# Kernel tuning notes

Hardware: AMD Instinct MI355X
Metric: run time of the kernel (lower is better)

## Reference

```python
import jax, jax.numpy as jnp
import numpy as np

U = 8192        # unique source nodes this hop
E = 200000      # candidate paths (edges)
D = 768         # node feature dim (== hidden, GIN residual requires it)
DE = 50         # edge one-hot dim
O = 768         # output dim
BN_EPS = 1e-5


def setup_inputs() -> dict:
    key = jax.random.key(0)
    ks = jax.random.split(key, 10)
    inp = {
        "x_src_unique": jax.random.normal(ks[0], (U, D), dtype=jnp.float32),
        "unique_src_to_process_indices": jnp.arange(U, dtype=jnp.int64),
        "path_source_indices_global": jax.random.randint(ks[1], (E,), 0, U).astype(jnp.int64),
        "path_target_node_features": jax.random.normal(ks[2], (E, D), dtype=jnp.float32),
        "path_edge_features": jax.random.normal(ks[3], (E, DE), dtype=jnp.float32),
        # edge_transform_linear: Linear(D+DE, H) with bias
        "W_edge": jax.random.normal(ks[4], (D, D + DE), dtype=jnp.float32) * (1.0 / np.sqrt(D + DE)),
        "b_edge": jnp.zeros((D,), dtype=jnp.float32),
        # MLP: two bias-free linears with BatchNorm1d between
        "W1": jax.random.normal(ks[5], (D, D), dtype=jnp.float32) * (1.0 / np.sqrt(D)),
        "W2": jax.random.normal(ks[6], (O, D), dtype=jnp.float32) * (1.0 / np.sqrt(D)),
        "bn_gamma": jnp.ones((D,), dtype=jnp.float32),
        "bn_beta": jnp.zeros((D,), dtype=jnp.float32),
        "eps_param": jnp.zeros((1,), dtype=jnp.float32),  # GIN eps (init_eps=0)
    }
    return inp


def reference(x_src_unique, unique_src_to_process_indices, path_source_indices_global,
              path_target_node_features, path_edge_features,
              W_edge, b_edge, W1, W2, bn_gamma, bn_beta, eps_param):
    # map global source ids -> local rows of x_src_unique (unique ids are sorted)
    local_idx = jnp.searchsorted(unique_src_to_process_indices, path_source_indices_global)

    # per-path message: relu(Linear([h_tgt ; e_onehot]))  -> [E, H]
    msg_in = jnp.concatenate([path_target_node_features, path_edge_features], axis=-1)
    msgs = jax.nn.relu(msg_in @ W_edge.T + b_edge)

    # scatter-sum messages to their source node  -> [U, H]
    agg = jax.ops.segment_sum(msgs, local_idx, num_segments=x_src_unique.shape[0])

    # GIN combine + MLP (BatchNorm1d in training mode, batch > 1)
    h = (1.0 + eps_param[0]) * x_src_unique + agg
    h1 = h @ W1.T                               # [U, H]
    mean = jnp.mean(h1, axis=0)
    var = jnp.var(h1, axis=0)                   # biased, matches torch BN normalization
    h1 = (h1 - mean) * jax.lax.rsqrt(var + BN_EPS) * bn_gamma + bn_beta
    h1 = jax.nn.relu(h1)
    return h1 @ W2.T                            # [U, O]
```

## Files before the change

kernel.cpp:

```cpp
#include <hip/hip_runtime.h>
#include <stdint.h>
#include <math.h>

typedef unsigned short u16;
typedef __attribute__((ext_vector_type(4))) float f32x4;
typedef __attribute__((ext_vector_type(8))) short s16x8;
typedef __attribute__((ext_vector_type(4))) int i32x4;

#define U_N 8192
#define E_N 200000
#define M_PAD 200192
#define D_N 768
#define DE_N 50
#define KP_E 832
#define NTI 13
#define BN_EPS 1e-5f

__device__ __forceinline__ u16 f2bf(float f) {
  union { float f; unsigned u; } v; v.f = f;
  return (u16)((v.u + 0x7fffu + ((v.u >> 16) & 1u)) >> 16);
}
__device__ __forceinline__ float bf2f(u16 v) {
  union { unsigned u; float f; } x; x.u = ((unsigned)v) << 16; return x.f;
}
__device__ __forceinline__ void gload16(const void* g, void* l) {
  __builtin_amdgcn_global_load_lds((const __attribute__((address_space(1))) void*)g,
                                   (__attribute__((address_space(3))) void*)l, 16, 0, 0);
}

__global__ void k_localidx(const int* __restrict__ uniq, const int* __restrict__ src,
                           int* __restrict__ lidx) {
  int e = blockIdx.x * 256 + threadIdx.x;
  if (e >= E_N) return;
  int v = src[e];
  int lo = 0, hi = U_N;
  while (lo < hi) { int mid = (lo + hi) >> 1; if (uniq[mid] < v) lo = mid + 1; else hi = mid; }
  lidx[e] = lo;
}

__global__ void k_hist(const int* __restrict__ lidx, int* __restrict__ counts) {
  int e = blockIdx.x * 256 + threadIdx.x;
  if (e < E_N) atomicAdd(&counts[lidx[e]], 1);
}

__global__ void k_scan(const int* __restrict__ counts, int* __restrict__ starts) {
  __shared__ int part[1024];
  const int t = threadIdx.x;
  const int base = t * 8;
  int loc[8]; int s = 0;
#pragma unroll
  for (int i = 0; i < 8; i++) { loc[i] = s; s += counts[base + i]; }
  part[t] = s; __syncthreads();
  for (int off = 1; off < 1024; off <<= 1) {
    int v = (t >= off) ? part[t - off] : 0;
    __syncthreads();
    part[t] += v;
    __syncthreads();
  }
  const int pre = (t == 0) ? 0 : part[t - 1];
#pragma unroll
  for (int i = 0; i < 8; i++) starts[base + i] = pre + loc[i];
  if (t == 1023) starts[8192] = pre + s;
}

__global__ void k_scatter(const int* __restrict__ lidx, const int* __restrict__ starts,
                          int* __restrict__ cursor, int* __restrict__ eord,
                          int* __restrict__ nsort) {
  int e = blockIdx.x * 256 + threadIdx.x;
  if (e >= E_N) return;
  int u = lidx[e];
  int pos = atomicAdd(&cursor[u], 1);
  eord[starts[u] + pos] = e;
  nsort[starts[u] + pos] = u;
}

__global__ __launch_bounds__(256)
void k_pack_q8(const float* __restrict__ tgt, const float* __restrict__ edg,
               const int* __restrict__ eord, char* __restrict__ Aq,
               float* __restrict__ sA) {
  const int row = blockIdx.x * 4 + (threadIdx.x >> 6);
  const int lane = threadIdx.x & 63;
  if (row >= E_N) return;
  const int e = eord[row];
  const int k0 = lane * 16;
  float v[16];
#pragma unroll
  for (int z = 0; z < 16; z++) v[z] = 0.f;
  if (k0 < D_N) {
    const f32x4* p = (const f32x4*)(tgt + (size_t)e * D_N + k0);
#pragma unroll
    for (int zz = 0; zz < 4; zz++) {
      const f32x4 f = p[zz];
#pragma unroll
      for (int b = 0; b < 4; b++) v[zz * 4 + b] = f[b];
    }
  } else if (k0 < KP_E) {
#pragma unroll
    for (int z = 0; z < 16; z++) {
      const int kk = k0 + z - D_N;
      v[z] = (kk < DE_N) ? edg[(size_t)e * DE_N + kk] : 0.f;
    }
  }
  float am = 0.f;
#pragma unroll
  for (int z = 0; z < 16; z++) am = fmaxf(am, fabsf(v[z]));
#pragma unroll
  for (int off = 32; off > 0; off >>= 1) am = fmaxf(am, __shfl_xor(am, off));
  am = fmaxf(am, 1e-8f);
  const float inv = 127.f / am;
  if (lane == 0) sA[row] = am / 127.f;
  if (k0 < KP_E) {
    int wq[4];
#pragma unroll
    for (int zz = 0; zz < 4; zz++) {
      int b0 = (int)rintf(fminf(fmaxf(v[zz*4+0] * inv, -127.f), 127.f));
      int b1 = (int)rintf(fminf(fmaxf(v[zz*4+1] * inv, -127.f), 127.f));
      int b2 = (int)rintf(fminf(fmaxf(v[zz*4+2] * inv, -127.f), 127.f));
      int b3 = (int)rintf(fminf(fmaxf(v[zz*4+3] * inv, -127.f), 127.f));
      wq[zz] = (b0 & 255) | ((b1 & 255) << 8) | ((b2 & 255) << 16) | (b3 << 24);
    }
    i32x4 out = {wq[0], wq[1], wq[2], wq[3]};
    *(i32x4*)(Aq + (size_t)row * KP_E + k0) = out;
  }
}

__global__ __launch_bounds__(256)
void k_convw_q8(const float* __restrict__ W, char* __restrict__ Wq,
                float* __restrict__ sW) {
  const int row = blockIdx.x * 4 + (threadIdx.x >> 6);
  const int lane = threadIdx.x & 63;
  if (row >= D_N) return;
  const int k0 = lane * 16;
  float v[16];
#pragma unroll
  for (int z = 0; z < 16; z++) v[z] = 0.f;
  if (k0 < KP_E) {
#pragma unroll
    for (int z = 0; z < 16; z++) {
      const int kk = k0 + z;
      v[z] = (kk < D_N + DE_N) ? W[(size_t)row * (D_N + DE_N) + kk] : 0.f;
    }
  }
  float am = 0.f;
#pragma unroll
  for (int z = 0; z < 16; z++) am = fmaxf(am, fabsf(v[z]));
#pragma unroll
  for (int off = 32; off > 0; off >>= 1) am = fmaxf(am, __shfl_xor(am, off));
  am = fmaxf(am, 1e-8f);
  const float inv = 127.f / am;
  if (lane == 0) sW[row] = am / 127.f;
  if (k0 < KP_E) {
    int wq[4];
#pragma unroll
    for (int zz = 0; zz < 4; zz++) {
      int b0 = (int)rintf(fminf(fmaxf(v[zz*4+0] * inv, -127.f), 127.f));
      int b1 = (int)rintf(fminf(fmaxf(v[zz*4+1] * inv, -127.f), 127.f));
      int b2 = (int)rintf(fminf(fmaxf(v[zz*4+2] * inv, -127.f), 127.f));
      int b3 = (int)rintf(fminf(fmaxf(v[zz*4+3] * inv, -127.f), 127.f));
      wq[zz] = (b0 & 255) | ((b1 & 255) << 8) | ((b2 & 255) << 16) | (b3 << 24);
    }
    i32x4 out = {wq[0], wq[1], wq[2], wq[3]};
    *(i32x4*)(Wq + (size_t)row * KP_E + k0) = out;
  }
}

__global__ void k_conv_w(const float* __restrict__ W, u16* __restrict__ Wb, int count) {
  int i = blockIdx.x * 256 + threadIdx.x;
  if (i < count) Wb[i] = f2bf(W[i]);
}

__global__ __launch_bounds__(512)
void gemm_edge7(const char* __restrict__ Aq, const char* __restrict__ Wq,
                const float* __restrict__ sA, const float* __restrict__ sW,
                const float* __restrict__ bias, const int* __restrict__ nsort,
                float* __restrict__ agg) {
  __shared__ char lds[139264];

  const int orig = blockIdx.x;
  const int xcd = orig & 7, i8_ = orig >> 3;
  const int wgid = (xcd < 2 ? xcd * 294 : 588 + (xcd - 2) * 293) + i8_;
  const int bm = (wgid / 3) * 256;
  const int bn = (wgid % 3) * 256;

  const int tid = threadIdx.x;
  const int w = tid >> 6, lane = tid & 63;
  const int wm = w >> 2, wn = w & 3;
  const int rl = lane & 15, K16 = lane >> 4;
  const int sws16 = (K16 ^ ((rl >> 1) & 3)) * 16;
  const int srow = lane >> 2;
  const int sslot = lane & 3;
  const int sg = sslot ^ ((srow >> 1) & 3);

  i32x4 acc[8][4] = {};

#define STAGE(T)                                                                        \
  {                                                                                     \
    const int b_ = (T) & 3;                                                             \
    const int k0_ = (T) * 64;                                                           \
    _Pragma("unroll")                                                                   \
    for (int q_ = 0; q_ < 2; ++q_) {                                                    \
      const int c_ = w * 2 + q_;                                                        \
      const int r_ = c_ * 16 + srow;                                                    \
      gload16(Aq + (size_t)(bm + r_) * KP_E + k0_ + sg * 16, lds + b_ * 16384 + c_ * 1024); \
    }                                                                                   \
    _Pragma("unroll")                                                                   \
    for (int q_ = 0; q_ < 2; ++q_) {                                                    \
      const int c_ = w * 2 + q_;                                                        \
      const int r_ = c_ * 16 + srow;                                                    \
      gload16(Wq + (size_t)(bn + r_) * KP_E + k0_ + sg * 16, lds + 65536 + b_ * 16384 + c_ * 1024); \
    }                                                                                   \
  }

#define COMPUTE(BB)                                                                     \
  {                                                                                     \
    const char* Ab = lds + (BB) * 16384;                                                \
    const char* Bb = lds + 65536 + (BB) * 16384;                                        \
    i32x4 bfr[4], af[4];                                                                \
    _Pragma("unroll")                                                                   \
    for (int j_ = 0; j_ < 4; ++j_)                                                      \
      bfr[j_] = *(const i32x4*)(Bb + (wn * 64 + j_ * 16 + rl) * 64 + sws16);            \
    _Pragma("unroll")                                                                   \
    for (int i_ = 0; i_ < 4; ++i_)                                                      \
      af[i_] = *(const i32x4*)(Ab + (wm * 128 + i_ * 16 + rl) * 64 + sws16);            \
    __builtin_amdgcn_s_setprio(1);                                                      \
    _Pragma("unroll")                                                                   \
    for (int i_ = 0; i_ < 4; ++i_)                                                      \
      _Pragma("unroll")                                                                 \
      for (int j_ = 0; j_ < 4; ++j_)                                                    \
        acc[i_][j_] = __builtin_amdgcn_mfma_i32_16x16x64_i8(af[i_], bfr[j_],            \
                                                            acc[i_][j_], 0, 0, 0);     \
    __builtin_amdgcn_s_setprio(0);                                                      \
    _Pragma("unroll")                                                                   \
    for (int i_ = 0; i_ < 4; ++i_)                                                      \
      af[i_] = *(const i32x4*)(Ab + (wm * 128 + (4 + i_) * 16 + rl) * 64 + sws16);      \
    __builtin_amdgcn_s_setprio(1);                                                      \
    _Pragma("unroll")                                                                   \
    for (int i_ = 0; i_ < 4; ++i_)                                                      \
      _Pragma("unroll")                                                                 \
      for (int j_ = 0; j_ < 4; ++j_)                                                    \
        acc[4 + i_][j_] = __builtin_amdgcn_mfma_i32_16x16x64_i8(af[i_], bfr[j_],        \
                                                                acc[4 + i_][j_], 0, 0, 0); \
    __builtin_amdgcn_s_setprio(0);                                                      \
  }

#define VMC(n)  asm volatile("s_waitcnt vmcnt(" #n ")" ::: "memory")
#define BAR()   __builtin_amdgcn_s_barrier()

  STAGE(0)
  STAGE(1)
  STAGE(2)

  for (int t = 0; t < NTI - 3; ++t) {
    VMC(8);
    BAR();
    asm volatile("" ::: "memory");
    STAGE(t + 3)
    COMPUTE(t & 3)
  }
  VMC(8); BAR(); asm volatile("" ::: "memory");
  COMPUTE(2)
  VMC(4); BAR(); asm volatile("" ::: "memory");
  COMPUTE(3)
  VMC(0); BAR(); asm volatile("" ::: "memory");
  COMPUTE(0)

#undef STAGE
#undef COMPUTE

  BAR();

  u16* tile = (u16*)lds;
  int* nseg = (int*)(lds + 137216);
  float* sAl = (float*)(lds + 138240);
  for (int i = tid; i < 256; i += 512) {
    nseg[i] = nsort[bm + i];
    sAl[i] = sA[bm + i];
  }
  __syncthreads();

  const int rq = (lane >> 4) * 4;
  const int cl = lane & 15;
#pragma unroll
  for (int j = 0; j < 4; ++j) {
    const int col16 = wn * 64 + j * 16 + cl;
    const float swn = sW[bn + col16];
    const float bj = bias[bn + col16];
#pragma unroll
    for (int mf = 0; mf < 8; ++mf) {
      const int r0 = wm * 128 + mf * 16 + rq;
#pragma unroll
      for (int q = 0; q < 4; ++q) {
        const int r = r0 + q;
        const float v = fmaf((float)acc[mf][j][q], sAl[r] * swn, bj);
        tile[r * 268 + col16] = f2bf(v > 0.f ? v : 0.f);
      }
    }
  }
  __syncthreads();

  const int col = tid & 255;
  const int rbase = (tid >> 8) * 128;
  float s = 0.f;
  int cur = -1;
  for (int r = 0; r < 128; ++r) {
    const int nd = nseg[rbase + r];
    const float v = bf2f(tile[(rbase + r) * 268 + col]);
    if (nd != cur) {
      if (cur >= 0) atomicAdd(&agg[(size_t)cur * D_N + bn + col], s);
      s = 0.f;
      cur = nd;
    }
    if (nd >= 0) s += v;
  }
  if (cur >= 0) atomicAdd(&agg[(size_t)cur * D_N + bn + col], s);

#undef VMC
#undef BAR
}

__global__ void k_build_h(const float* __restrict__ x, const float* __restrict__ agg,
                          const float* __restrict__ epsp, u16* __restrict__ hbf) {
  int i = blockIdx.x * 256 + threadIdx.x;
  if (i >= U_N * D_N) return;
  float h = (1.f + epsp[0]) * x[i] + agg[i];
  hbf[i] = f2bf(h);
}

__global__ __launch_bounds__(256)
void gemm_bf16_g(const u16* __restrict__ A, const u16* __restrict__ B,
                 float* __restrict__ C, int ntn, int K) {
  __shared__ u16 As[128 * 64];
  __shared__ u16 Bs[128 * 64];
  const int bm = (blockIdx.x / ntn) * 128;
  const int bn = (blockIdx.x % ntn) * 128;
  const int t = threadIdx.x;
  const int wave = t >> 6, lane = t & 63;
  const int wr = (wave & 1) * 64, wc = (wave >> 1) * 64;
  const int srow = lane >> 3, scol = (lane & 7) * 8;
  const int rl = lane & 15, kl = (lane >> 4) * 8;
  const int N = ntn * 128;
  f32x4 acc[4][4] = {};
  for (int k0 = 0; k0 < K; k0 += 64) {
#pragma unroll
    for (int q = 0; q < 4; q++) {
      const int c = wave * 4 + q;
      const int row = c * 8 + srow;
      gload16(A + (size_t)(bm + row) * K + k0 + scol, As + c * 512);
      gload16(B + (size_t)(bn + row) * K + k0 + scol, Bs + c * 512);
    }
    __syncthreads();
#pragma unroll
    for (int ks = 0; ks < 2; ks++) {
      s16x8 af[4], bfr[4];
#pragma unroll
      for (int i = 0; i < 4; i++) af[i] = *(const s16x8*)&As[(wr + i * 16 + rl) * 64 + ks * 32 + kl];
#pragma unroll
      for (int j = 0; j < 4; j++) bfr[j] = *(const s16x8*)&Bs[(wc + j * 16 + rl) * 64 + ks * 32 + kl];
#pragma unroll
      for (int i = 0; i < 4; i++)
#pragma unroll
        for (int j = 0; j < 4; j++)
          acc[i][j] = __builtin_amdgcn_mfma_f32_16x16x32_bf16(af[i], bfr[j], acc[i][j], 0, 0, 0);
    }
    __syncthreads();
  }
  const int cl = lane & 15, rq = (lane >> 4) * 4;
#pragma unroll
  for (int i = 0; i < 4; i++)
#pragma unroll
    for (int j = 0; j < 4; j++) {
      const int n = bn + wc + j * 16 + cl;
      const int r = bm + wr + i * 16 + rq;
#pragma unroll
      for (int q = 0; q < 4; q++)
        C[(size_t)(r + q) * N + n] = acc[i][j][q];
    }
}

__global__ void k_bnstats(const float* __restrict__ h1, float* __restrict__ ssum,
                          float* __restrict__ ssq) {
  const int cchunk = blockIdx.x % 3;
  const int rchunk = blockIdx.x / 3;
  const int c = cchunk * 256 + threadIdx.x;
  const int r0 = rchunk * 256;
  float s = 0.f, s2 = 0.f;
  for (int r = r0; r < r0 + 256; r++) {
    float v = h1[(size_t)r * D_N + c];
    s += v; s2 += v * v;
  }
  atomicAdd(&ssum[c], s);
  atomicAdd(&ssq[c], s2);
}

__global__ void k_bnfinal(const float* __restrict__ ssum, const float* __restrict__ ssq,
                          const float* __restrict__ gamma, const float* __restrict__ beta,
                          float* __restrict__ scale, float* __restrict__ shift) {
  int c = blockIdx.x * 256 + threadIdx.x;
  if (c >= D_N) return;
  double mean = (double)ssum[c] / (double)U_N;
  double var = (double)ssq[c] / (double)U_N - mean * mean;
  float sc = (float)((double)gamma[c] / sqrt(var + (double)BN_EPS));
  scale[c] = sc;
  shift[c] = beta[c] - (float)mean * sc;
}

__global__ void k_bnapply(const float* __restrict__ h1, const float* __restrict__ scale,
                          const float* __restrict__ shift, u16* __restrict__ h2) {
  int i = blockIdx.x * 256 + threadIdx.x;
  if (i >= U_N * D_N) return;
  int c = i % D_N;
  float v = h1[i] * scale[c] + shift[c];
  h2[i] = f2bf(v > 0.f ? v : 0.f);
}

extern "C" void kernel_launch(void* const* d_in, const int* in_sizes, int n_in,
                              void* d_out, int out_size, void* d_ws, size_t ws_size,
                              hipStream_t stream) {
  const float* x     = (const float*)d_in[0];
  const int*   uniq  = (const int*)d_in[1];
  const int*   srcg  = (const int*)d_in[2];
  const float* tgt   = (const float*)d_in[3];
  const float* edg   = (const float*)d_in[4];
  const float* Wedge = (const float*)d_in[5];
  const float* bedge = (const float*)d_in[6];
  const float* W1    = (const float*)d_in[7];
  const float* W2    = (const float*)d_in[8];
  const float* gamma = (const float*)d_in[9];
  const float* beta  = (const float*)d_in[10];
  const float* epsp  = (const float*)d_in[11];
  float* out = (float*)d_out;
  char* ws = (char*)d_ws;

  char*  Aq    = (char*) (ws + 0);
  float* agg   = (float*)(ws + 166559744ull);
  float* h1    = (float*)(ws + 191725568ull);
  u16*   hbf   = (u16*)  (ws + 216891392ull);
  u16*   h2b   = (u16*)  (ws + 229474304ull);
  char*  Wq    = (char*) (ws + 242057216ull);
  u16*   w1b   = (u16*)  (ws + 242696192ull);
  u16*   w2b   = (u16*)  (ws + 243875840ull);
  float* sA    = (float*)(ws + 245055488ull);
  float* sW    = (float*)(ws + 245856256ull);
  int*   lidx  = (int*)  (ws + 245860352ull);
  int*   eord  = (int*)  (ws + 246660352ull);
  int*   nsort = (int*)  (ws + 247460352ull);
  int*   counts= (int*)  (ws + 248261120ull);
  int*   cursor= (int*)  (ws + 248293888ull);
  int*   starts= (int*)  (ws + 248326656ull);
  float* ssum  = (float*)(ws + 248359680ull);
  float* ssq   = (float*)(ws + 248362752ull);
  float* scale = (float*)(ws + 248365824ull);
  float* shift = (float*)(ws + 248368896ull);

  hipMemsetAsync(counts, 0, 65536, stream);
  hipMemsetAsync(ssum, 0, 2 * D_N * 4, stream);
  hipMemsetAsync(agg, 0, (size_t)U_N * D_N * 4, stream);
  hipMemsetAsync(nsort + E_N, 0xFF, (M_PAD - E_N) * 4, stream);

  k_convw_q8<<<D_N / 4, 256, 0, stream>>>(Wedge, Wq, sW);
  k_conv_w<<<(D_N * D_N + 255) / 256, 256, 0, stream>>>(W1, w1b, D_N * D_N);
  k_conv_w<<<(D_N * D_N + 255) / 256, 256, 0, stream>>>(W2, w2b, D_N * D_N);

  k_localidx<<<(E_N + 255) / 256, 256, 0, stream>>>(uniq, srcg, lidx);
  k_hist<<<(E_N + 255) / 256, 256, 0, stream>>>(lidx, counts);
  k_scan<<<1, 1024, 0, stream>>>(counts, starts);
  k_scatter<<<(E_N + 255) / 256, 256, 0, stream>>>(lidx, starts, cursor, eord, nsort);

  k_pack_q8<<<E_N / 4, 256, 0, stream>>>(tgt, edg, eord, Aq, sA);

  gemm_edge7<<<782 * 3, 512, 0, stream>>>(Aq, Wq, sA, sW, bedge, nsort, agg);

  k_build_h<<<(U_N * D_N + 255) / 256, 256, 0, stream>>>(x, agg, epsp, hbf);

  gemm_bf16_g<<<(U_N / 128) * 6, 256, 0, stream>>>(hbf, w1b, h1, 6, D_N);

  k_bnstats<<<96, 256, 0, stream>>>(h1, ssum, ssq);
  k_bnfinal<<<3, 256, 0, stream>>>(ssum, ssq, gamma, beta, scale, shift);
  k_bnapply<<<(U_N * D_N + 255) / 256, 256, 0, stream>>>(h1, scale, shift, h2b);

  gemm_bf16_g<<<(U_N / 128) * 6, 256, 0, stream>>>(h2b, w2b, out, 6, D_N);
}
```

Before: 583.6 us.

## Retile int8 edge GEMM to K=128 double buffer; fuse BN stats into first MLP GEMM

The edge GEMM now pads K to 896 and stages 128-wide K tiles with two LDS buffers instead of four 64-wide buffers. That halves the iteration count but adds padding work and shortens prefetch depth. Separately, a new GEMM for the first MLP layer writes h1 as bf16 and accumulates the BatchNorm column sums and squares via atomics in its epilogue. This removes the separate bnstats pass and halves h1 traffic in bnapply, at the cost of some precision in h1 and extra atomics.

After: 569.1 us. -2.5%, faster.

```diff
diff --git a/kernel.cpp b/kernel.cpp
--- a/kernel.cpp
+++ b/kernel.cpp
@@ -12,8 +12,8 @@
 #define M_PAD 200192
 #define D_N 768
 #define DE_N 50
-#define KP_E 832
-#define NTI 13
+#define KP8 896
+#define NTI8 7
 #define BN_EPS 1e-5f
 
 __device__ __forceinline__ u16 f2bf(float f) {
@@ -94,7 +94,7 @@
 #pragma unroll
       for (int b = 0; b < 4; b++) v[zz * 4 + b] = f[b];
     }
-  } else if (k0 < KP_E) {
+  } else if (k0 < KP8) {
 #pragma unroll
     for (int z = 0; z < 16; z++) {
       const int kk = k0 + z - D_N;
@@ -109,7 +109,7 @@
   am = fmaxf(am, 1e-8f);
   const float inv = 127.f / am;
   if (lane == 0) sA[row] = am / 127.f;
-  if (k0 < KP_E) {
+  if (k0 < KP8) {
     int wq[4];
 #pragma unroll
     for (int zz = 0; zz < 4; zz++) {
@@ -120,7 +120,7 @@
       wq[zz] = (b0 & 255) | ((b1 & 255) << 8) | ((b2 & 255) << 16) | (b3 << 24);
     }
     i32x4 out = {wq[0], wq[1], wq[2], wq[3]};
-    *(i32x4*)(Aq + (size_t)row * KP_E + k0) = out;
+    *(i32x4*)(Aq + (size_t)row * KP8 + k0) = out;
   }
 }
 
@@ -134,7 +134,7 @@
   float v[16];
 #pragma unroll
   for (int z = 0; z < 16; z++) v[z] = 0.f;
-  if (k0 < KP_E) {
+  if (k0 < KP8) {
 #pragma unroll
     for (int z = 0; z < 16; z++) {
       const int kk = k0 + z;
@@ -149,7 +149,7 @@
   am = fmaxf(am, 1e-8f);
   const float inv = 127.f / am;
   if (lane == 0) sW[row] = am / 127.f;
-  if (k0 < KP_E) {
+  if (k0 < KP8) {
     int wq[4];
 #pragma unroll
     for (int zz = 0; zz < 4; zz++) {
@@ -160,7 +160,7 @@
       wq[zz] = (b0 & 255) | ((b1 & 255) << 8) | ((b2 & 255) << 16) | (b3 << 24);
     }
     i32x4 out = {wq[0], wq[1], wq[2], wq[3]};
-    *(i32x4*)(Wq + (size_t)row * KP_E + k0) = out;
+    *(i32x4*)(Wq + (size_t)row * KP8 + k0) = out;
   }
 }
 
@@ -170,7 +170,7 @@
 }
 
 __global__ __launch_bounds__(512)
-void gemm_edge7(const char* __restrict__ Aq, const char* __restrict__ Wq,
+void gemm_edge8(const char* __restrict__ Aq, const char* __restrict__ Wq,
                 const float* __restrict__ sA, const float* __restrict__ sW,
                 const float* __restrict__ bias, const int* __restrict__ nsort,
                 float* __restrict__ agg) {
@@ -186,42 +186,42 @@
   const int w = tid >> 6, lane = tid & 63;
   const int wm = w >> 2, wn = w & 3;
   const int rl = lane & 15, K16 = lane >> 4;
-  const int sws16 = (K16 ^ ((rl >> 1) & 3)) * 16;
-  const int srow = lane >> 2;
-  const int sslot = lane & 3;
-  const int sg = sslot ^ ((srow >> 1) & 3);
+  const int srr = lane >> 3;
+  const int ssrc = (lane & 7) ^ srr;
 
   i32x4 acc[8][4] = {};
 
-#define STAGE(T)                                                                        \
+#define STAGE8(T)                                                                       \
   {                                                                                     \
-    const int b_ = (T) & 3;                                                             \
-    const int k0_ = (T) * 64;                                                           \
-    _Pragma("unroll")                                                                   \
-    for (int q_ = 0; q_ < 2; ++q_) {                                                    \
-      const int c_ = w * 2 + q_;                                                        \
-      const int r_ = c_ * 16 + srow;                                                    \
-      gload16(Aq + (size_t)(bm + r_) * KP_E + k0_ + sg * 16, lds + b_ * 16384 + c_ * 1024); \
+    const int b_ = (T) & 1;                                                             \
+    const int k0_ = (T) * 128;                                                          \
+    _Pragma("unroll")                                                                   \
+    for (int c_ = 0; c_ < 4; ++c_) {                                                    \
+      const int cc_ = c_ * 8 + w;                                                       \
+      const int r_ = cc_ * 8 + srr;                                                     \
+      gload16(Aq + (size_t)(bm + r_) * KP8 + k0_ + ssrc * 16, lds + b_ * 32768 + cc_ * 1024); \
     }                                                                                   \
     _Pragma("unroll")                                                                   \
-    for (int q_ = 0; q_ < 2; ++q_) {                                                    \
-      const int c_ = w * 2 + q_;                                                        \
-      const int r_ = c_ * 16 + srow;                                                    \
-      gload16(Wq + (size_t)(bn + r_) * KP_E + k0_ + sg * 16, lds + 65536 + b_ * 16384 + c_ * 1024); \
+    for (int c_ = 0; c_ < 4; ++c_) {                                                    \
+      const int cc_ = c_ * 8 + w;                                                       \
+      const int r_ = cc_ * 8 + srr;                                                     \
+      gload16(Wq + (size_t)(bn + r_) * KP8 + k0_ + ssrc * 16, lds + 65536 + b_ * 32768 + cc_ * 1024); \
     }                                                                                   \
   }
 
-#define COMPUTE(BB)                                                                     \
+#define COMPUTE_H(BB, h_)                                                               \
   {                                                                                     \
-    const char* Ab = lds + (BB) * 16384;                                                \
-    const char* Bb = lds + 65536 + (BB) * 16384;                                        \
+    const char* Ab = lds + (BB) * 32768;                                                \
+    const char* Bb = lds + 65536 + (BB) * 32768;                                        \
+    const int sb_ = (h_) * 4 + K16;                                                     \
+    const int sw_ = (sb_ ^ (rl & 7)) * 16;                                              \
     i32x4 bfr[4], af[4];                                                                \
     _Pragma("unroll")                                                                   \
     for (int j_ = 0; j_ < 4; ++j_)                                                      \
-      bfr[j_] = *(const i32x4*)(Bb + (wn * 64 + j_ * 16 + rl) * 64 + sws16);            \
+      bfr[j_] = *(const i32x4*)(Bb + (wn * 64 + j_ * 16 + rl) * 128 + sw_);             \
     _Pragma("unroll")                                                                   \
     for (int i_ = 0; i_ < 4; ++i_)                                                      \
-      af[i_] = *(const i32x4*)(Ab + (wm * 128 + i_ * 16 + rl) * 64 + sws16);            \
+      af[i_] = *(const i32x4*)(Ab + (wm * 128 + i_ * 16 + rl) * 128 + sw_);             \
     __builtin_amdgcn_s_setprio(1);                                                      \
     _Pragma("unroll")                                                                   \
     for (int i_ = 0; i_ < 4; ++i_)                                                      \
@@ -232,7 +232,7 @@
     __builtin_amdgcn_s_setprio(0);                                                      \
     _Pragma("unroll")                                                                   \
     for (int i_ = 0; i_ < 4; ++i_)                                                      \
-      af[i_] = *(const i32x4*)(Ab + (wm * 128 + (4 + i_) * 16 + rl) * 64 + sws16);      \
+      af[i_] = *(const i32x4*)(Ab + (wm * 128 + (4 + i_) * 16 + rl) * 128 + sw_);       \
     __builtin_amdgcn_s_setprio(1);                                                      \
     _Pragma("unroll")                                                                   \
     for (int i_ = 0; i_ < 4; ++i_)                                                      \
@@ -246,26 +246,25 @@
 #define VMC(n)  asm volatile("s_waitcnt vmcnt(" #n ")" ::: "memory")
 #define BAR()   __builtin_amdgcn_s_barrier()
 
-  STAGE(0)
-  STAGE(1)
-  STAGE(2)
-
-  for (int t = 0; t < NTI - 3; ++t) {
+  STAGE8(0)
+  for (int t = 0; t < NTI8 - 1; ++t) {
+    BAR();
+    STAGE8(t + 1)
     VMC(8);
     BAR();
     asm volatile("" ::: "memory");
-    STAGE(t + 3)
-    COMPUTE(t & 3)
-  }
-  VMC(8); BAR(); asm volatile("" ::: "memory");
-  COMPUTE(2)
-  VMC(4); BAR(); asm volatile("" ::: "memory");
-  COMPUTE(3)
-  VMC(0); BAR(); asm volatile("" ::: "memory");
-  COMPUTE(0)
-
-#undef STAGE
-#undef COMPUTE
+    COMPUTE_H(t & 1, 0)
+    COMPUTE_H(t & 1, 1)
+  }
+  BAR();
+  VMC(0);
+  BAR();
+  asm volatile("" ::: "memory");
+  COMPUTE_H(0, 0)
+  COMPUTE_H(0, 1)
+
+#undef STAGE8
+#undef COMPUTE_H
 
   BAR();
 
@@ -324,6 +323,64 @@
   if (i >= U_N * D_N) return;
   float h = (1.f + epsp[0]) * x[i] + agg[i];
   hbf[i] = f2bf(h);
+}
+
+__global__ __launch_bounds__(256)
+void gemm_h1(const u16* __restrict__ A, const u16* __restrict__ B,
+             u16* __restrict__ h1b, float* __restrict__ ssum, float* __restrict__ ssq) {
+  __shared__ u16 As[128 * 64];
+  __shared__ u16 Bs[128 * 64];
+  const int bm = (blockIdx.x / 6) * 128;
+  const int bn = (blockIdx.x % 6) * 128;
+  const int t = threadIdx.x;
+  const int wave = t >> 6, lane = t & 63;
+  const int wr = (wave & 1) * 64, wc = (wave >> 1) * 64;
+  const int srow = lane >> 3, scol = (lane & 7) * 8;
+  const int rl = lane & 15, kl = (lane >> 4) * 8;
+  f32x4 acc[4][4] = {};
+  for (int k0 = 0; k0 < D_N; k0 += 64) {
+#pragma unroll
+    for (int q = 0; q < 4; q++) {
+      const int c = wave * 4 + q;
+      const int row = c * 8 + srow;
+      gload16(A + (size_t)(bm + row) * D_N + k0 + scol, As + c * 512);
+      gload16(B + (size_t)(bn + row) * D_N + k0 + scol, Bs + c * 512);
+    }
+    __syncthreads();
+#pragma unroll
+    for (int ks = 0; ks < 2; ks++) {
+      s16x8 af[4], bfr[4];
+#pragma unroll
+      for (int i = 0; i < 4; i++) af[i] = *(const s16x8*)&As[(wr + i * 16 + rl) * 64 + ks * 32 + kl];
+#pragma unroll
+      for (int j = 0; j < 4; j++) bfr[j] = *(const s16x8*)&Bs[(wc + j * 16 + rl) * 64 + ks * 32 + kl];
+#pragma unroll
+      for (int i = 0; i < 4; i++)
+#pragma unroll
+        for (int j = 0; j < 4; j++)
+          acc[i][j] = __builtin_amdgcn_mfma_f32_16x16x32_bf16(af[i], bfr[j], acc[i][j], 0, 0, 0);
+    }
+    __syncthreads();
+  }
+  const int cl = lane & 15, rq = (lane >> 4) * 4;
+#pragma unroll
+  for (int j = 0; j < 4; j++) {
+    const int n = bn + wc + j * 16 + cl;
+    float cs = 0.f, cq = 0.f;
+#pragma unroll
+    for (int i = 0; i < 4; i++) {
+      const int r = bm + wr + i * 16 + rq;
+#pragma unroll
+      for (int q = 0; q < 4; q++) {
+        const float v = acc[i][j][q];
+        cs += v; cq += v * v;
+        h1b[(size_t)(r + q) * D_N + n] = f2bf(v);
+      }
+    }
+    cs += __shfl_xor(cs, 16); cq += __shfl_xor(cq, 16);
+    cs += __shfl_xor(cs, 32); cq += __shfl_xor(cq, 32);
+    if (lane < 16) { atomicAdd(&ssum[n], cs); atomicAdd(&ssq[n], cq); }
+  }
 }
 
 __global__ __launch_bounds__(256)
@@ -377,21 +434,6 @@
     }
 }
 
-__global__ void k_bnstats(const float* __restrict__ h1, float* __restrict__ ssum,
-                          float* __restrict__ ssq) {
-  const int cchunk = blockIdx.x % 3;
-  const int rchunk = blockIdx.x / 3;
-  const int c = cchunk * 256 + threadIdx.x;
-  const int r0 = rchunk * 256;
-  float s = 0.f, s2 = 0.f;
-  for (int r = r0; r < r0 + 256; r++) {
-    float v = h1[(size_t)r * D_N + c];
-    s += v; s2 += v * v;
-  }
-  atomicAdd(&ssum[c], s);
-  atomicAdd(&ssq[c], s2);
-}
-
 __global__ void k_bnfinal(const float* __restrict__ ssum, const float* __restrict__ ssq,
                           const float* __restrict__ gamma, const float* __restrict__ beta,
                           float* __restrict__ scale, float* __restrict__ shift) {
@@ -404,12 +446,12 @@
   shift[c] = beta[c] - (float)mean * sc;
 }
 
-__global__ void k_bnapply(const float* __restrict__ h1, const float* __restrict__ scale,
+__global__ void k_bnapply(const u16* __restrict__ h1b, const float* __restrict__ scale,
                           const float* __restrict__ shift, u16* __restrict__ h2) {
   int i = blockIdx.x * 256 + threadIdx.x;
   if (i >= U_N * D_N) return;
   int c = i % D_N;
-  float v = h1[i] * scale[c] + shift[c];
+  float v = bf2f(h1b[i]) * scale[c] + shift[c];
   h2[i] = f2bf(v > 0.f ? v : 0.f);
 }
 
@@ -432,25 +474,25 @@
   char* ws = (char*)d_ws;
 
   char*  Aq    = (char*) (ws + 0);
-  float* agg   = (float*)(ws + 166559744ull);
-  float* h1    = (float*)(ws + 191725568ull);
-  u16*   hbf   = (u16*)  (ws + 216891392ull);
-  u16*   h2b   = (u16*)  (ws + 229474304ull);
-  char*  Wq    = (char*) (ws + 242057216ull);
-  u16*   w1b   = (u16*)  (ws + 242696192ull);
-  u16*   w2b   = (u16*)  (ws + 243875840ull);
-  float* sA    = (float*)(ws + 245055488ull);
-  float* sW    = (float*)(ws + 245856256ull);
-  int*   lidx  = (int*)  (ws + 245860352ull);
-  int*   eord  = (int*)  (ws + 246660352ull);
-  int*   nsort = (int*)  (ws + 247460352ull);
-  int*   counts= (int*)  (ws + 248261120ull);
-  int*   cursor= (int*)  (ws + 248293888ull);
-  int*   starts= (int*)  (ws + 248326656ull);
-  float* ssum  = (float*)(ws + 248359680ull);
-  float* ssq   = (float*)(ws + 248362752ull);
-  float* scale = (float*)(ws + 248365824ull);
-  float* shift = (float*)(ws + 248368896ull);
+  float* agg   = (float*)(ws + 179372032ull);
+  u16*   h1b   = (u16*)  (ws + 204537856ull);
+  u16*   hbf   = (u16*)  (ws + 217120768ull);
+  u16*   h2b   = (u16*)  (ws + 229703680ull);
+  char*  Wq    = (char*) (ws + 242286592ull);
+  u16*   w1b   = (u16*)  (ws + 242974720ull);
+  u16*   w2b   = (u16*)  (ws + 244154368ull);
+  float* sA    = (float*)(ws + 245334016ull);
+  float* sW    = (float*)(ws + 246134784ull);
+  int*   lidx  = (int*)  (ws + 246138880ull);
+  int*   eord  = (int*)  (ws + 246938880ull);
+  int*   nsort = (int*)  (ws + 247738880ull);
+  int*   counts= (int*)  (ws + 248539648ull);
+  int*   cursor= (int*)  (ws + 248572416ull);
+  int*   starts= (int*)  (ws + 248605184ull);
+  float* ssum  = (float*)(ws + 248638208ull);
+  float* ssq   = (float*)(ws + 248641280ull);
+  float* scale = (float*)(ws + 248644352ull);
+  float* shift = (float*)(ws + 248647424ull);
 
   hipMemsetAsync(counts, 0, 65536, stream);
   hipMemsetAsync(ssum, 0, 2 * D_N * 4, stream);
@@ -468,15 +510,14 @@
 
   k_pack_q8<<<E_N / 4, 256, 0, stream>>>(tgt, edg, eord, Aq, sA);
 
-  gemm_edge7<<<782 * 3, 512, 0, stream>>>(Aq, Wq, sA, sW, bedge, nsort, agg);
+  gemm_edge8<<<782 * 3, 512, 0, stream>>>(Aq, Wq, sA, sW, bedge, nsort, agg);
 
   k_build_h<<<(U_N * D_N + 255) / 256, 256, 0, stream>>>(x, agg, epsp, hbf);
 
-  gemm_bf16_g<<<(U_N / 128) * 6, 256, 0, stream>>>(hbf, w1b, h1, 6, D_N);
-
-  k_bnstats<<<96, 256, 0, stream>>>(h1, ssum, ssq);
+  gemm_h1<<<(U_N / 128) * 6, 256, 0, stream>>>(hbf, w1b, h1b, ssum, ssq);
+
   k_bnfinal<<<3, 256, 0, stream>>>(ssum, ssq, gamma, beta, scale, shift);
-  k_bnapply<<<(U_N * D_N + 255) / 256, 256, 0, stream>>>(h1, scale, shift, h2b);
+  k_bnapply<<<(U_N * D_N + 255) / 256, 256, 0, stream>>>(h1b, scale, shift, h2b);
 
   gemm_bf16_g<<<(U_N / 128) * 6, 256, 0, stream>>>(h2b, w2b, out, 6, D_N);
 }
```
